# Performance work log

Measured on AMD Instinct MI355X. Metric: run time of the kernel, lower is better.

The kernel has to match this reference:

```python
import jax, jax.numpy as jnp
import numpy as np

B, N, F_DIM = 32, 1024, 128
ALPHA = 0.2        # LeakyReLU negative slope
PAD = -9e15        # pad_sequence padding value in the original
DENSITY = 0.05


def setup_inputs() -> dict:
    key = jax.random.key(0)
    k1, k2, k3 = jax.random.split(key, 3)
    # sparse 0/1 adjacency with self-loops so every node has degree >= 1
    adj = (jax.random.uniform(k1, (B, N, N)) < DENSITY).astype(jnp.float32)
    eye = jnp.eye(N, dtype=jnp.float32)[None, :, :]
    adj = jnp.maximum(adj, eye)
    feats = jax.random.normal(k2, (B, N, F_DIM), dtype=jnp.float32)
    # xavier_uniform with leaky_relu gain on a [2F, 1]
    gain = float(np.sqrt(2.0 / (1.0 + ALPHA ** 2)))
    bound = gain * float(np.sqrt(6.0 / (2 * F_DIM + 1)))
    a = jax.random.uniform(k3, (2 * F_DIM, 1), minval=-bound, maxval=bound,
                           dtype=jnp.float32)
    return {"batch_graphs": adj, "batch_features": feats, "a": a}


def reference(batch_graphs, batch_features, a):
    # e_ij = LeakyReLU([h_i || h_j] @ a) decomposes as (h_i @ a1) + (h_j @ a2)
    s_src = batch_features @ a[:F_DIM, 0]   # [B, N] contribution of node i
    s_dst = batch_features @ a[F_DIM:, 0]   # [B, N] contribution of neighbor j
    e = s_src[:, :, None] + s_dst[:, None, :]            # [B, N, N]
    e = jnp.where(e >= 0, e, ALPHA * e)                   # LeakyReLU
    mask = batch_graphs == 1
    e = jnp.where(mask, e, PAD)                           # pad non-edges like pad_sequence
    att = jax.nn.softmax(e, axis=-1)                      # segmented softmax over neighbors
    att = jnp.where(mask, att, 0.0)                       # scatter back only real edges
    return att
```

## Files before the change

### kernel.cpp

```cpp
#include <hip/hip_runtime.h>
#include <hip/hip_bf16.h>
#include <stdint.h>

#define B_DIM 32
#define N_DIM 1024
#define F_DIM 128
#define ALPHA 0.2f
#define NROWS (B_DIM * N_DIM)
#define TAIL_ROWS 128
#define MAIN_ROWS (NROWS - TAIL_ROWS)
#define SCORE_BYTES ((size_t)(2 * NROWS) * sizeof(float))

typedef float          vf4 __attribute__((ext_vector_type(4)));
typedef unsigned short vh4 __attribute__((ext_vector_type(4)));
typedef unsigned int   vu4 __attribute__((ext_vector_type(4)));

__device__ __forceinline__ unsigned short f32_to_bf16_bits(float f) {
    union { __hip_bfloat16 h; unsigned short u; } cvt;
    cvt.h = __float2bfloat16(f);
    return cvt.u;
}

__device__ __forceinline__ bool probe_is_f32(const void* adj) {
    return *(const uint32_t*)adj == 0x3F800000u;
}

template <bool F32>
__device__ __forceinline__ float* score_base(void* out) {
    const size_t out_bytes = (size_t)NROWS * N_DIM * (F32 ? 4 : 2);
    return (float*)((char*)out + out_bytes - SCORE_BYTES);
}

template <bool F32>
__device__ __forceinline__ void scores_body(
    const void* __restrict__ feats_v, const void* __restrict__ a_v, void* out)
{
    float* base  = score_base<F32>(out);
    float* s_src = base;
    float* s_dst = base + NROWS;

    const int wid  = threadIdx.x >> 6;
    const int lane = threadIdx.x & 63;
    const int row  = blockIdx.x * 4 + wid;
    const int f0   = lane * 2;

    float x0, x1, a10, a11, a20, a21;
    if (F32) {
        const float* fp = (const float*)feats_v + (size_t)row * F_DIM + f0;
        const float* ap = (const float*)a_v;
        x0 = fp[0]; x1 = fp[1];
        a10 = ap[f0];         a11 = ap[f0 + 1];
        a20 = ap[F_DIM + f0]; a21 = ap[F_DIM + f0 + 1];
    } else {
        const __hip_bfloat16* fp = (const __hip_bfloat16*)feats_v + (size_t)row * F_DIM + f0;
        const __hip_bfloat16* ap = (const __hip_bfloat16*)a_v;
        x0  = __bfloat162float(fp[0]);           x1  = __bfloat162float(fp[1]);
        a10 = __bfloat162float(ap[f0]);          a11 = __bfloat162float(ap[f0 + 1]);
        a20 = __bfloat162float(ap[F_DIM + f0]);  a21 = __bfloat162float(ap[F_DIM + f0 + 1]);
    }

    float v1 = x0 * a10 + x1 * a11;
    float v2 = x0 * a20 + x1 * a21;
    #pragma unroll
    for (int off = 32; off > 0; off >>= 1) {
        v1 += __shfl_down(v1, off, 64);
        v2 += __shfl_down(v2, off, 64);
    }
    if (lane == 0) { s_src[row] = v1; s_dst[row] = v2; }
}

__global__ __launch_bounds__(256) void scores_kernel(
    const void* __restrict__ adj, const void* __restrict__ feats,
    const void* __restrict__ a, void* out)
{
    if (probe_is_f32(adj)) scores_body<true>(feats, a, out);
    else                   scores_body<false>(feats, a, out);
}

template <bool F32>
__device__ __forceinline__ void wave_softmax_row(
    const void* __restrict__ adj_v, void* __restrict__ out_v,
    int row, float ssrc, const float* __restrict__ sdst )
{
    const int lane = threadIdx.x & 63;

    float p[16];
    uint32_t vmask = 0;
    float lmax = -1e30f;

    #pragma unroll
    for (int c = 0; c < 4; ++c) {
        const int idx = c * 64 + lane;
        const vf4 sd = ((const vf4*)sdst)[idx];
        bool v[4];
        if (F32) {
            const vu4 av = ((const vu4*)((const float*)adj_v + (size_t)row * N_DIM))[idx];
            v[0] = av.x != 0u; v[1] = av.y != 0u; v[2] = av.z != 0u; v[3] = av.w != 0u;
        } else {
            const vh4 av = ((const vh4*)((const __hip_bfloat16*)adj_v + (size_t)row * N_DIM))[idx];
            v[0] = av.x != 0; v[1] = av.y != 0; v[2] = av.z != 0; v[3] = av.w != 0;
        }
        const float sdk[4] = {sd.x, sd.y, sd.z, sd.w};
        #pragma unroll
        for (int k = 0; k < 4; ++k) {
            float t = ssrc + sdk[k];
            t = (t >= 0.0f) ? t : ALPHA * t;
            p[c * 4 + k] = t;
            if (v[k]) { lmax = fmaxf(lmax, t); vmask |= 1u << (c * 4 + k); }
        }
    }

    #pragma unroll
    for (int off = 1; off < 64; off <<= 1)
        lmax = fmaxf(lmax, __shfl_xor(lmax, off, 64));

    float lsum = 0.0f;
    #pragma unroll
    for (int i = 0; i < 16; ++i) {
        p[i] = (vmask >> i) & 1 ? __expf(p[i] - lmax) : 0.0f;
        lsum += p[i];
    }
    #pragma unroll
    for (int off = 1; off < 64; off <<= 1)
        lsum += __shfl_xor(lsum, off, 64);
    const float inv = 1.0f / lsum;

    #pragma unroll
    for (int c = 0; c < 4; ++c) {
        const int idx = c * 64 + lane;
        if (F32) {
            vf4 o;
            o.x = p[c*4+0] * inv; o.y = p[c*4+1] * inv;
            o.z = p[c*4+2] * inv; o.w = p[c*4+3] * inv;
            __builtin_nontemporal_store(o,
                ((vf4*)((float*)out_v + (size_t)row * N_DIM)) + idx);
        } else {
            vh4 o;
            o.x = f32_to_bf16_bits(p[c*4+0] * inv);
            o.y = f32_to_bf16_bits(p[c*4+1] * inv);
            o.z = f32_to_bf16_bits(p[c*4+2] * inv);
            o.w = f32_to_bf16_bits(p[c*4+3] * inv);
            __builtin_nontemporal_store(o,
                ((vh4*)((__hip_bfloat16*)out_v + (size_t)row * N_DIM)) + idx);
        }
    }
}

template <bool F32>
__device__ __forceinline__ void main_body(const void* __restrict__ adj_v, void* out_v)
{
    const int wid = threadIdx.x >> 6;
    const int row = blockIdx.x * 4 + wid;
    const int b   = row >> 10;

    const float* base = score_base<F32>(out_v);
    const float  ssrc = base[row];
    const float* sdst = base + NROWS + (size_t)b * N_DIM;

    wave_softmax_row<F32>(adj_v, out_v, row, ssrc, sdst);
}

__global__ __launch_bounds__(256) void main_kernel(
    const void* __restrict__ adj, void* out)
{
    if (probe_is_f32(adj)) main_body<true>(adj, out);
    else                   main_body<false>(adj, out);
}

template <bool F32>
__device__ __forceinline__ void tail_body(const void* __restrict__ adj_v, void* out_v)
{
    __shared__ float sdst_sh[N_DIM];
    __shared__ float ssrc_sh[TAIL_ROWS];

    const int tid  = threadIdx.x;
    const float* base = score_base<F32>(out_v);

    sdst_sh[tid] = base[NROWS + (B_DIM - 1) * N_DIM + tid];
    if (tid < TAIL_ROWS) ssrc_sh[tid] = base[MAIN_ROWS + tid];
    __syncthreads();

    const int wid = tid >> 6;
    #pragma unroll
    for (int r = 0; r < TAIL_ROWS / 16; ++r) {
        const int rr  = wid * (TAIL_ROWS / 16) + r;
        const int row = MAIN_ROWS + rr;
        wave_softmax_row<F32>(adj_v, out_v, row, ssrc_sh[rr], sdst_sh);
    }
}

__global__ __launch_bounds__(1024) void tail_kernel(
    const void* __restrict__ adj, void* out)
{
    if (probe_is_f32(adj)) tail_body<true>(adj, out);
    else                   tail_body<false>(adj, out);
}

extern "C" void kernel_launch(void* const* d_in, const int* in_sizes, int n_in,
                              void* d_out, int out_size, void* d_ws, size_t ws_size,
                              hipStream_t stream) {
    const void* adj   = d_in[0];
    const void* feats = d_in[1];
    const void* a     = d_in[2];
    (void)d_ws; (void)ws_size;

    scores_kernel<<<NROWS / 4, 256, 0, stream>>>(adj, feats, a, d_out);
    main_kernel<<<MAIN_ROWS / 4, 256, 0, stream>>>(adj, d_out);
    tail_kernel<<<1, 1024, 0, stream>>>(adj, d_out);
}
```

Before: 266.3 us.

## Spread tail rows over many blocks recomputing scores, use regular stores

The tail kernel used to run as one 1024-thread block that handled 128 rows serially, reading scores kept at the end of the output buffer. It now launches 32 blocks of 256 threads. Each block recomputes the last batch's destination scores and its own rows' source scores straight from the features, then runs the softmax for its rows. This replaces a serialized single-block tail with parallel work, at the cost of redundant dot products in every block. Output stores also switch from nontemporal to regular stores, which changes cache behavior for the large output write.

```diff
diff --git a/kernel.cpp b/kernel.cpp
--- a/kernel.cpp
+++ b/kernel.cpp
@@ -132,16 +132,14 @@
             vf4 o;
             o.x = p[c*4+0] * inv; o.y = p[c*4+1] * inv;
             o.z = p[c*4+2] * inv; o.w = p[c*4+3] * inv;
-            __builtin_nontemporal_store(o,
-                ((vf4*)((float*)out_v + (size_t)row * N_DIM)) + idx);
+            ((vf4*)((float*)out_v + (size_t)row * N_DIM))[idx] = o;
         } else {
             vh4 o;
             o.x = f32_to_bf16_bits(p[c*4+0] * inv);
             o.y = f32_to_bf16_bits(p[c*4+1] * inv);
             o.z = f32_to_bf16_bits(p[c*4+2] * inv);
             o.w = f32_to_bf16_bits(p[c*4+3] * inv);
-            __builtin_nontemporal_store(o,
-                ((vh4*)((__hip_bfloat16*)out_v + (size_t)row * N_DIM)) + idx);
+            ((vh4*)((__hip_bfloat16*)out_v + (size_t)row * N_DIM))[idx] = o;
         }
     }
 }
@@ -168,32 +166,71 @@
 }
 
 template <bool F32>
-__device__ __forceinline__ void tail_body(const void* __restrict__ adj_v, void* out_v)
+__device__ __forceinline__ void tail_body(
+    const void* __restrict__ adj_v, const void* __restrict__ feats_v,
+    const void* __restrict__ a_v, void* __restrict__ out_v)
 {
     __shared__ float sdst_sh[N_DIM];
-    __shared__ float ssrc_sh[TAIL_ROWS];
 
     const int tid  = threadIdx.x;
-    const float* base = score_base<F32>(out_v);
-
-    sdst_sh[tid] = base[NROWS + (B_DIM - 1) * N_DIM + tid];
-    if (tid < TAIL_ROWS) ssrc_sh[tid] = base[MAIN_ROWS + tid];
+    const int wid  = tid >> 6;
+    const int lane = tid & 63;
+    const int b    = B_DIM - 1;
+    const int row  = MAIN_ROWS + blockIdx.x * 4 + wid;
+
+    #pragma unroll
+    for (int k = 0; k < 4; ++k) {
+        const int j = tid * 4 + k;
+        float acc = 0.0f;
+        if (F32) {
+            const vf4* fp = (const vf4*)((const float*)feats_v + ((size_t)b * N_DIM + j) * F_DIM);
+            const vf4* ap = (const vf4*)((const float*)a_v + F_DIM);
+            #pragma unroll 8
+            for (int f = 0; f < F_DIM / 4; ++f) {
+                const vf4 x = fp[f], w = ap[f];
+                acc += x.x * w.x + x.y * w.y + x.z * w.z + x.w * w.w;
+            }
+        } else {
+            const __hip_bfloat16* fp = (const __hip_bfloat16*)feats_v + ((size_t)b * N_DIM + j) * F_DIM;
+            const __hip_bfloat16* ap = (const __hip_bfloat16*)a_v + F_DIM;
+            #pragma unroll 8
+            for (int f = 0; f < F_DIM; ++f)
+                acc += __bfloat162float(fp[f]) * __bfloat162float(ap[f]);
+        }
+        sdst_sh[j] = acc;
+    }
+
+    float ssrc;
+    {
+        const int f0 = lane * 2;
+        float x0, x1, a0, a1;
+        if (F32) {
+            const float* fp = (const float*)feats_v + (size_t)row * F_DIM + f0;
+            const float* ap = (const float*)a_v;
+            x0 = fp[0]; x1 = fp[1]; a0 = ap[f0]; a1 = ap[f0 + 1];
+        } else {
+            const __hip_bfloat16* fp = (const __hip_bfloat16*)feats_v + (size_t)row * F_DIM + f0;
+            const __hip_bfloat16* ap = (const __hip_bfloat16*)a_v;
+            x0 = __bfloat162float(fp[0]); x1 = __bfloat162float(fp[1]);
+            a0 = __bfloat162float(ap[f0]); a1 = __bfloat162float(ap[f0 + 1]);
+        }
+        float v = x0 * a0 + x1 * a1;
+        #pragma unroll
+        for (int off = 32; off > 0; off >>= 1)
+            v += __shfl_down(v, off, 64);
+        ssrc = __shfl(v, 0, 64);
+    }
     __syncthreads();
 
-    const int wid = tid >> 6;
-    #pragma unroll
-    for (int r = 0; r < TAIL_ROWS / 16; ++r) {
-        const int rr  = wid * (TAIL_ROWS / 16) + r;
-        const int row = MAIN_ROWS + rr;
-        wave_softmax_row<F32>(adj_v, out_v, row, ssrc_sh[rr], sdst_sh);
-    }
-}
-
-__global__ __launch_bounds__(1024) void tail_kernel(
-    const void* __restrict__ adj, void* out)
-{
-    if (probe_is_f32(adj)) tail_body<true>(adj, out);
-    else                   tail_body<false>(adj, out);
+    wave_softmax_row<F32>(adj_v, out_v, row, ssrc, sdst_sh);
+}
+
+__global__ __launch_bounds__(256) void tail_kernel(
+    const void* __restrict__ adj, const void* __restrict__ feats,
+    const void* __restrict__ a, void* __restrict__ out)
+{
+    if (probe_is_f32(adj)) tail_body<true>(adj, feats, a, out);
+    else                   tail_body<false>(adj, feats, a, out);
 }
 
 extern "C" void kernel_launch(void* const* d_in, const int* in_sizes, int n_in,
@@ -206,5 +243,5 @@
 
     scores_kernel<<<NROWS / 4, 256, 0, stream>>>(adj, feats, a, d_out);
     main_kernel<<<MAIN_ROWS / 4, 256, 0, stream>>>(adj, d_out);
-    tail_kernel<<<1, 1024, 0, stream>>>(adj, d_out);
-}
+    tail_kernel<<<TAIL_ROWS / 4, 256, 0, stream>>>(adj, feats, a, d_out);
+}
```

Result: no change. 262.2 us (-1.6%).
